# Kernel optimization log

Measured on AMD Instinct MI355X. Metric: run time of the kernel, lower is better.

The kernel has to match this reference:

```python
import jax, jax.numpy as jnp
import numpy as np

TEMP = 5.0

def setup_inputs() -> dict:
    key = jax.random.key(0)
    k1, k2 = jax.random.split(key)
    text_features = jax.random.normal(k1, (512, 512), dtype=jnp.float32)   # [A, D]
    video_features = jax.random.normal(k2, (512, 32, 512), dtype=jnp.float32)  # [B, V, D]
    return {"text_features": text_features, "video_features": video_features}

def reference(text_features, video_features):
    # scores: [A, B, V] = text (A,D) x video (B,V,D)
    v_weight = jnp.einsum('ad,bvd->abv', text_features, video_features)
    v_weight = jax.nn.softmax(v_weight / TEMP, axis=-1)
    # pooled: [A, B, D]
    v_feat = jnp.einsum('abv,bvd->abd', v_weight, video_features)
    return v_feat
```

## Files before the change

### kernel.cpp

```cpp
#include <hip/hip_runtime.h>

typedef _Float16 f16x8 __attribute__((ext_vector_type(8)));
typedef float f32x4 __attribute__((ext_vector_type(4)));

#define NA 512
#define NB 512
#define NV 32
#define ND 512
#define NBV (NB * NV)

__global__ __launch_bounds__(256) void k_vt(const float* __restrict__ video,
                                            _Float16* __restrict__ vt) {
  __shared__ _Float16 tile[ND * NV];
  int b = blockIdx.x, t = threadIdx.x;
  const float* vb = video + (size_t)b * NV * ND;
  int v = t >> 3, dc = (t & 7) * 64;
  for (int i = 0; i < 16; ++i) {
    f32x4 x = *(const f32x4*)(vb + v * ND + dc + i * 4);
    int d = dc + i * 4;
    tile[(d + 0) * NV + v] = (_Float16)x[0];
    tile[(d + 1) * NV + v] = (_Float16)x[1];
    tile[(d + 2) * NV + v] = (_Float16)x[2];
    tile[(d + 3) * NV + v] = (_Float16)x[3];
  }
  __syncthreads();
  f16x8* dst = (f16x8*)(vt + (size_t)b * ND * NV);
  const f16x8* src = (const f16x8*)tile;
  for (int i = 0; i < 8; ++i) dst[i * 256 + t] = src[i * 256 + t];
}

__device__ inline void stage8(const float* __restrict__ g, _Float16* l) {
  f32x4 x = *(const f32x4*)g;
  f32x4 y = *(const f32x4*)(g + 4);
  f16x8 h;
  h[0] = (_Float16)x[0]; h[1] = (_Float16)x[1];
  h[2] = (_Float16)x[2]; h[3] = (_Float16)x[3];
  h[4] = (_Float16)y[0]; h[5] = (_Float16)y[1];
  h[6] = (_Float16)y[2]; h[7] = (_Float16)y[3];
  *(f16x8*)l = h;
}

__device__ inline int swz(int row, int ch) {
  return row * 32 + ((ch ^ ((row >> 1) & 3)) * 8);
}

__global__ __launch_bounds__(256) void k_scores(const float* __restrict__ text,
                                                const float* __restrict__ video,
                                                _Float16* __restrict__ W) {
  __shared__ _Float16 As[128 * 32];
  __shared__ _Float16 Bs[128 * 32];
  int t = threadIdx.x;
  int m0 = blockIdx.y * 128, n0 = blockIdx.x * 128;
  int w = t >> 6, lane = t & 63, ln = lane & 15, q = lane >> 4;
  int wm = (w >> 1) * 64, wn = (w & 1) * 64;
  int r0 = t >> 2, c0 = t & 3;
  int r1 = (t + 256) >> 2;
  f32x4 acc[4][4];
  for (int i = 0; i < 4; ++i)
    for (int j = 0; j < 4; ++j) acc[i][j] = (f32x4){0.f, 0.f, 0.f, 0.f};

  for (int kk = 0; kk < 16; ++kk) {
    int k0 = kk * 32;
    __syncthreads();
    stage8(text + (size_t)(m0 + r0) * ND + k0 + c0 * 8, As + swz(r0, c0));
    stage8(text + (size_t)(m0 + r1) * ND + k0 + c0 * 8, As + swz(r1, c0));
    stage8(video + (size_t)(n0 + r0) * ND + k0 + c0 * 8, Bs + swz(r0, c0));
    stage8(video + (size_t)(n0 + r1) * ND + k0 + c0 * 8, Bs + swz(r1, c0));
    __syncthreads();
    f16x8 af[4], bf[4];
    for (int mt = 0; mt < 4; ++mt)
      af[mt] = *(const f16x8*)(As + swz(wm + mt * 16 + ln, q));
    for (int nt = 0; nt < 4; ++nt)
      bf[nt] = *(const f16x8*)(Bs + swz(wn + nt * 16 + ln, q));
    for (int mt = 0; mt < 4; ++mt)
      for (int nt = 0; nt < 4; ++nt)
        acc[mt][nt] = __builtin_amdgcn_mfma_f32_16x16x32_f16(af[mt], bf[nt],
                                                             acc[mt][nt], 0, 0, 0);
  }

  const float invT = 0.2f;
  for (int mt = 0; mt < 4; ++mt) {
    for (int g = 0; g < 2; ++g) {
      for (int r = 0; r < 4; ++r) {
        float v0 = acc[mt][2 * g][r] * invT;
        float v1 = acc[mt][2 * g + 1][r] * invT;
        float mx = fmaxf(v0, v1);
        for (int msk = 1; msk < 16; msk <<= 1)
          mx = fmaxf(mx, __shfl_xor(mx, msk, 16));
        float p0 = __expf(v0 - mx), p1 = __expf(v1 - mx);
        float s = p0 + p1;
        for (int msk = 1; msk < 16; msk <<= 1)
          s += __shfl_xor(s, msk, 16);
        float inv = 1.0f / s;
        int a = m0 + wm + mt * 16 + q * 4 + r;
        int col = n0 + wn + g * 32 + ln;
        W[(size_t)a * NBV + col] = (_Float16)(p0 * inv);
        W[(size_t)a * NBV + col + 16] = (_Float16)(p1 * inv);
      }
    }
  }
}

__global__ __launch_bounds__(256) void k_pool(const _Float16* __restrict__ W,
                                              const _Float16* __restrict__ vt,
                                              float* __restrict__ out) {
  int a0 = blockIdx.x * 64, b = blockIdx.y;
  int t = threadIdx.x, w = t >> 6, lane = t & 63, ln = lane & 15, q = lane >> 4;
  f16x8 af[4];
  for (int mt = 0; mt < 4; ++mt)
    af[mt] = *(const f16x8*)(W + (size_t)(a0 + mt * 16 + ln) * NBV + b * NV + q * 8);
  const _Float16* vtb = vt + (size_t)b * ND * NV;
  for (int nt = 0; nt < 8; ++nt) {
    int d0 = w * 128 + nt * 16;
    f16x8 bf = *(const f16x8*)(vtb + (d0 + ln) * NV + q * 8);
    for (int mt = 0; mt < 4; ++mt) {
      f32x4 c = (f32x4){0.f, 0.f, 0.f, 0.f};
      c = __builtin_amdgcn_mfma_f32_16x16x32_f16(af[mt], bf, c, 0, 0, 0);
      int abase = a0 + mt * 16 + q * 4;
      for (int r = 0; r < 4; ++r)
        out[((size_t)(abase + r) * NB + b) * ND + d0 + ln] = c[r];
    }
  }
}

extern "C" void kernel_launch(void* const* d_in, const int* in_sizes, int n_in,
                              void* d_out, int out_size, void* d_ws, size_t ws_size,
                              hipStream_t stream) {
  const float* text = (const float*)d_in[0];
  const float* video = (const float*)d_in[1];
  float* out = (float*)d_out;
  _Float16* VT = (_Float16*)d_ws;
  _Float16* W = (_Float16*)((char*)d_ws + (size_t)NB * ND * NV * sizeof(_Float16));
  k_vt<<<dim3(NB), 256, 0, stream>>>(video, VT);
  k_scores<<<dim3(NBV / 128, NA / 128), 256, 0, stream>>>(text, video, W);
  k_pool<<<dim3(NA / 64, NB), 256, 0, stream>>>(W, VT, out);
}
```

Measured before the change: 679.4 us.

## Pre-convert inputs to fp16, shrink score tile, restructure pooling for vector stores

The prep kernel now also writes fp16 copies of text and video, so the scores GEMM loads half-width data instead of re-reading and converting fp32 in every tile. The scores tile shrinks from 128x128 to 64x128, doubling the number of blocks. The pooling kernel is reorganised so each 512-thread block covers 8 batches and 64 rows, swapping MFMA operands so each lane writes contiguous f32x4 output chunks. This costs extra workspace and an extra pass writing fp16 copies.

```diff
diff --git a/kernel.cpp b/kernel.cpp
--- a/kernel.cpp
+++ b/kernel.cpp
@@ -1,6 +1,7 @@
 #include <hip/hip_runtime.h>
 
 typedef _Float16 f16x8 __attribute__((ext_vector_type(8)));
+typedef _Float16 f16x4 __attribute__((ext_vector_type(4)));
 typedef float f32x4 __attribute__((ext_vector_type(4)));
 
 #define NA 512
@@ -9,8 +10,11 @@
 #define ND 512
 #define NBV (NB * NV)
 
-__global__ __launch_bounds__(256) void k_vt(const float* __restrict__ video,
-                                            _Float16* __restrict__ vt) {
+__global__ __launch_bounds__(256) void k_prep(const float* __restrict__ text,
+                                              const float* __restrict__ video,
+                                              _Float16* __restrict__ Tf,
+                                              _Float16* __restrict__ Vf,
+                                              _Float16* __restrict__ VT) {
   __shared__ _Float16 tile[ND * NV];
   int b = blockIdx.x, t = threadIdx.x;
   const float* vb = video + (size_t)b * NV * ND;
@@ -23,63 +27,69 @@
     tile[(d + 2) * NV + v] = (_Float16)x[2];
     tile[(d + 3) * NV + v] = (_Float16)x[3];
   }
+  for (int i = 0; i < 16; ++i) {
+    int off = i * 1024 + t * 4;
+    f32x4 x = *(const f32x4*)(vb + off);
+    f16x4 h;
+    h[0] = (_Float16)x[0]; h[1] = (_Float16)x[1];
+    h[2] = (_Float16)x[2]; h[3] = (_Float16)x[3];
+    *(f16x4*)(Vf + (size_t)b * (NV * ND) + off) = h;
+  }
+  if (b < 256) {
+    int idx = (b * 256 + t) * 4;
+    f32x4 x = *(const f32x4*)(text + idx);
+    f16x4 h;
+    h[0] = (_Float16)x[0]; h[1] = (_Float16)x[1];
+    h[2] = (_Float16)x[2]; h[3] = (_Float16)x[3];
+    *(f16x4*)(Tf + idx) = h;
+  }
   __syncthreads();
-  f16x8* dst = (f16x8*)(vt + (size_t)b * ND * NV);
+  f16x8* dst = (f16x8*)(VT + (size_t)b * ND * NV);
   const f16x8* src = (const f16x8*)tile;
   for (int i = 0; i < 8; ++i) dst[i * 256 + t] = src[i * 256 + t];
-}
-
-__device__ inline void stage8(const float* __restrict__ g, _Float16* l) {
-  f32x4 x = *(const f32x4*)g;
-  f32x4 y = *(const f32x4*)(g + 4);
-  f16x8 h;
-  h[0] = (_Float16)x[0]; h[1] = (_Float16)x[1];
-  h[2] = (_Float16)x[2]; h[3] = (_Float16)x[3];
-  h[4] = (_Float16)y[0]; h[5] = (_Float16)y[1];
-  h[6] = (_Float16)y[2]; h[7] = (_Float16)y[3];
-  *(f16x8*)l = h;
 }
 
 __device__ inline int swz(int row, int ch) {
   return row * 32 + ((ch ^ ((row >> 1) & 3)) * 8);
 }
 
-__global__ __launch_bounds__(256) void k_scores(const float* __restrict__ text,
-                                                const float* __restrict__ video,
+__global__ __launch_bounds__(256) void k_scores(const _Float16* __restrict__ Tf,
+                                                const _Float16* __restrict__ Vf,
                                                 _Float16* __restrict__ W) {
-  __shared__ _Float16 As[128 * 32];
+  __shared__ _Float16 As[64 * 32];
   __shared__ _Float16 Bs[128 * 32];
   int t = threadIdx.x;
-  int m0 = blockIdx.y * 128, n0 = blockIdx.x * 128;
+  int m0 = blockIdx.y * 64, n0 = blockIdx.x * 128;
   int w = t >> 6, lane = t & 63, ln = lane & 15, q = lane >> 4;
-  int wm = (w >> 1) * 64, wn = (w & 1) * 64;
-  int r0 = t >> 2, c0 = t & 3;
-  int r1 = (t + 256) >> 2;
-  f32x4 acc[4][4];
-  for (int i = 0; i < 4; ++i)
+  int wm = (w >> 1) * 32, wn = (w & 1) * 64;
+  int ra = t >> 2, ca = t & 3;
+  int rb = t >> 1, cb = (t & 1) * 2;
+  const _Float16* tA = Tf + (size_t)(m0 + ra) * ND + ca * 8;
+  const _Float16* tB = Vf + (size_t)(n0 + rb) * ND + cb * 8;
+  f32x4 acc[2][4];
+  for (int i = 0; i < 2; ++i)
     for (int j = 0; j < 4; ++j) acc[i][j] = (f32x4){0.f, 0.f, 0.f, 0.f};
 
   for (int kk = 0; kk < 16; ++kk) {
     int k0 = kk * 32;
     __syncthreads();
-    stage8(text + (size_t)(m0 + r0) * ND + k0 + c0 * 8, As + swz(r0, c0));
-    stage8(text + (size_t)(m0 + r1) * ND + k0 + c0 * 8, As + swz(r1, c0));
-    stage8(video + (size_t)(n0 + r0) * ND + k0 + c0 * 8, Bs + swz(r0, c0));
-    stage8(video + (size_t)(n0 + r1) * ND + k0 + c0 * 8, Bs + swz(r1, c0));
+    *(f16x8*)(As + swz(ra, ca)) = *(const f16x8*)(tA + k0);
+    *(f16x8*)(Bs + swz(rb, cb)) = *(const f16x8*)(tB + k0);
+    *(f16x8*)(Bs + swz(rb, cb + 1)) = *(const f16x8*)(tB + k0 + 8);
     __syncthreads();
-    f16x8 af[4], bf[4];
-    for (int mt = 0; mt < 4; ++mt)
+    f16x8 af[2], bf[4];
+    for (int mt = 0; mt < 2; ++mt)
       af[mt] = *(const f16x8*)(As + swz(wm + mt * 16 + ln, q));
     for (int nt = 0; nt < 4; ++nt)
       bf[nt] = *(const f16x8*)(Bs + swz(wn + nt * 16 + ln, q));
-    for (int mt = 0; mt < 4; ++mt)
+    for (int mt = 0; mt < 2; ++mt)
       for (int nt = 0; nt < 4; ++nt)
         acc[mt][nt] = __builtin_amdgcn_mfma_f32_16x16x32_f16(af[mt], bf[nt],
                                                              acc[mt][nt], 0, 0, 0);
   }
 
   const float invT = 0.2f;
-  for (int mt = 0; mt < 4; ++mt) {
+  for (int mt = 0; mt < 2; ++mt) {
     for (int g = 0; g < 2; ++g) {
       for (int r = 0; r < 4; ++r) {
         float v0 = acc[mt][2 * g][r] * invT;
@@ -101,24 +111,30 @@
   }
 }
 
-__global__ __launch_bounds__(256) void k_pool(const _Float16* __restrict__ W,
-                                              const _Float16* __restrict__ vt,
+__global__ __launch_bounds__(512) void k_pool(const _Float16* __restrict__ W,
+                                              const _Float16* __restrict__ VT,
                                               float* __restrict__ out) {
-  int a0 = blockIdx.x * 64, b = blockIdx.y;
-  int t = threadIdx.x, w = t >> 6, lane = t & 63, ln = lane & 15, q = lane >> 4;
-  f16x8 af[4];
-  for (int mt = 0; mt < 4; ++mt)
-    af[mt] = *(const f16x8*)(W + (size_t)(a0 + mt * 16 + ln) * NBV + b * NV + q * 8);
-  const _Float16* vtb = vt + (size_t)b * ND * NV;
-  for (int nt = 0; nt < 8; ++nt) {
-    int d0 = w * 128 + nt * 16;
-    f16x8 bf = *(const f16x8*)(vtb + (d0 + ln) * NV + q * 8);
-    for (int mt = 0; mt < 4; ++mt) {
-      f32x4 c = (f32x4){0.f, 0.f, 0.f, 0.f};
-      c = __builtin_amdgcn_mfma_f32_16x16x32_f16(af[mt], bf, c, 0, 0, 0);
-      int abase = a0 + mt * 16 + q * 4;
-      for (int r = 0; r < 4; ++r)
-        out[((size_t)(abase + r) * NB + b) * ND + d0 + ln] = c[r];
+  int t = threadIdx.x;
+  int w = t >> 6, lane = t & 63, ln = lane & 15, q = lane >> 4;
+  int b0 = blockIdx.x * 8, a0 = blockIdx.y * 64;
+  int d0 = w * 64;
+  const _Float16* Wbase = W + (size_t)(a0 + ln) * NBV + b0 * NV + q * 8;
+  for (int ib = 0; ib < 8; ++ib) {
+    const _Float16* vtb =
+        VT + ((size_t)(b0 + ib) * ND + d0 + ln) * NV + q * 8;
+    f16x8 wf[4], vf[4];
+    for (int nt = 0; nt < 4; ++nt)
+      wf[nt] = *(const f16x8*)(Wbase + (size_t)nt * 16 * NBV + ib * NV);
+    for (int mt = 0; mt < 4; ++mt)
+      vf[mt] = *(const f16x8*)(vtb + mt * 16 * NV);
+    for (int nt = 0; nt < 4; ++nt) {
+      for (int mt = 0; mt < 4; ++mt) {
+        f32x4 c = (f32x4){0.f, 0.f, 0.f, 0.f};
+        c = __builtin_amdgcn_mfma_f32_16x16x32_f16(vf[mt], wf[nt], c, 0, 0, 0);
+        float* dst = out + ((size_t)(a0 + nt * 16 + ln) * NB + b0 + ib) * ND +
+                     d0 + mt * 16 + q * 4;
+        *(f32x4*)dst = c;
+      }
     }
   }
 }
@@ -129,9 +145,12 @@
   const float* text = (const float*)d_in[0];
   const float* video = (const float*)d_in[1];
   float* out = (float*)d_out;
-  _Float16* VT = (_Float16*)d_ws;
-  _Float16* W = (_Float16*)((char*)d_ws + (size_t)NB * ND * NV * sizeof(_Float16));
-  k_vt<<<dim3(NB), 256, 0, stream>>>(video, VT);
-  k_scores<<<dim3(NBV / 128, NA / 128), 256, 0, stream>>>(text, video, W);
-  k_pool<<<dim3(NA / 64, NB), 256, 0, stream>>>(W, VT, out);
+  _Float16* ws = (_Float16*)d_ws;
+  _Float16* VT = ws;
+  _Float16* W  = ws + (size_t)8 * 1024 * 1024;
+  _Float16* Vf = ws + (size_t)16 * 1024 * 1024;
+  _Float16* Tf = ws + (size_t)24 * 1024 * 1024;
+  k_prep<<<dim3(NB), 256, 0, stream>>>(text, video, Tf, Vf, VT);
+  k_scores<<<dim3(NBV / 128, NA / 64), 256, 0, stream>>>(Tf, Vf, W);
+  k_pool<<<dim3(NB / 8, NA / 64), 512, 0, stream>>>(W, VT, out);
 }
```

After: 633.1 us. 1.07x faster.
